# Performance work log

Hardware: AMD Instinct MI355X
Metric: run time of the kernel (lower is better)

Reference implementation:

```python
import jax, jax.numpy as jnp
import numpy as np


def setup_inputs() -> dict:
    key = jax.random.key(0)
    k1, k2 = jax.random.split(key)
    B, H, W, C = 16, 1024, 1024, 3
    image = jax.random.normal(k1, (B, H, W, C), dtype=jnp.float32)
    flow = jax.random.normal(k2, (B, H, W, 2), dtype=jnp.float32)
    return {"image": image, "flow": flow}


def reference(image, flow):
    # Backward warp: out(p) = bilinear_sample(image, p + flow(p)).
    # NOTE: the original build() swaps width/height (width=shape[1], height=shape[2]);
    # this is only consistent for square images (H == W), which we assume here.
    B, H, W, C = image.shape
    grid_x = jnp.arange(W, dtype=jnp.float32)[None, None, :]  # [1,1,W]
    grid_y = jnp.arange(H, dtype=jnp.float32)[None, :, None]  # [1,H,1]
    x = grid_x + flow[..., 0]  # [B,H,W]
    y = grid_y + flow[..., 1]
    # normalize to [-1,1] then back (faithful to original round-trip)
    x = 0.5 * (2.0 * (x / W - 0.5) + 1.0) * W
    y = 0.5 * (2.0 * (y / H - 0.5) + 1.0) * H
    # corner indices (tf.cast truncates toward zero, as does astype(int32))
    x0 = x.astype(jnp.int32)
    x1 = x0 + 1
    y0 = y.astype(jnp.int32)
    y1 = y0 + 1
    x0 = jnp.clip(x0, 0, W - 1)
    x1 = jnp.clip(x1, 0, W - 1)
    y0 = jnp.clip(y0, 0, H - 1)
    y1 = jnp.clip(y1, 0, H - 1)
    # flat gather indices into [B*H*W, C] image, matching the 4 tf.gather calls
    base = (jnp.arange(B, dtype=jnp.int32) * (H * W))[:, None, None]  # [B,1,1]
    flat_img = image.reshape(B * H * W, C)
    ia = (base + y0 * W + x0).reshape(-1)
    ib = (base + y1 * W + x0).reshape(-1)
    ic = (base + y0 * W + x1).reshape(-1)
    idd = (base + y1 * W + x1).reshape(-1)
    pa = flat_img[ia]  # [B*H*W, C]
    pb = flat_img[ib]
    pc = flat_img[ic]
    pd = flat_img[idd]
    # bilinear blend weights from clipped corner coords (as in original)
    x0f = x0.astype(jnp.float32).reshape(-1)
    x1f = x1.astype(jnp.float32).reshape(-1)
    y0f = y0.astype(jnp.float32).reshape(-1)
    y1f = y1.astype(jnp.float32).reshape(-1)
    xf = x.reshape(-1)
    yf = y.reshape(-1)
    wa = ((x1f - xf) * (y1f - yf))[:, None]
    wb = ((x1f - xf) * (yf - y0f))[:, None]
    wc = ((xf - x0f) * (y1f - yf))[:, None]
    wd = ((xf - x0f) * (yf - y0f))[:, None]
    out = wa * pa + wb * pb + wc * pc + wd * pd
    return out.reshape(B, H, W, C)
```

## Files before the change

kernel.cpp:

```cpp
#include <hip/hip_runtime.h>


__global__ __launch_bounds__(256) void backwarp_kernel(
    const float* __restrict__ image,
    const float* __restrict__ flow,
    float* __restrict__ out,
    int B, int H, int W) {
  int idx = blockIdx.x * blockDim.x + threadIdx.x;
  int total = B * H * W;
  if (idx >= total) return;

  int w  = idx % W;
  int hw = idx / W;
  int h  = hw % H;
  int b  = hw / H;

  float2 f = *reinterpret_cast<const float2*>(flow + (size_t)idx * 2);

  float Wf = (float)W, Hf = (float)H;
  float x = (float)w + f.x;
  float y = (float)h + f.y;
  x = 0.5f * (2.0f * (x / Wf - 0.5f) + 1.0f) * Wf;
  y = 0.5f * (2.0f * (y / Hf - 0.5f) + 1.0f) * Hf;

  int x0 = (int)x;
  int y0 = (int)y;
  int x1 = x0 + 1;
  int y1 = y0 + 1;
  x0 = min(max(x0, 0), W - 1);
  x1 = min(max(x1, 0), W - 1);
  y0 = min(max(y0, 0), H - 1);
  y1 = min(max(y1, 0), H - 1);

  float x0f = (float)x0, x1f = (float)x1;
  float y0f = (float)y0, y1f = (float)y1;
  float wa = (x1f - x) * (y1f - y);
  float wb = (x1f - x) * (y - y0f);
  float wc = (x - x0f) * (y1f - y);
  float wd = (x - x0f) * (y - y0f);

  size_t plane = (size_t)b * H * W;
  const float* pa = image + (plane + (size_t)y0 * W + x0) * 3;
  const float* pb = image + (plane + (size_t)y1 * W + x0) * 3;
  const float* pc = image + (plane + (size_t)y0 * W + x1) * 3;
  const float* pd = image + (plane + (size_t)y1 * W + x1) * 3;

  float* o = out + (size_t)idx * 3;
#pragma unroll
  for (int c = 0; c < 3; ++c) {
    o[c] = wa * pa[c] + wb * pb[c] + wc * pc[c] + wd * pd[c];
  }
}

extern "C" void kernel_launch(void* const* d_in, const int* in_sizes, int n_in,
                              void* d_out, int out_size, void* d_ws, size_t ws_size,
                              hipStream_t stream) {
  const float* image = (const float*)d_in[0];
  const float* flow  = (const float*)d_in[1];
  float* out = (float*)d_out;

  const int B = 16, H = 1024, W = 1024;
  int total = B * H * W;
  int block = 256;
  int grid = (total + block - 1) / block;
  backwarp_kernel<<<grid, block, 0, stream>>>(image, flow, out, B, H, W);
}
```

Measured before the change: 157.1 us.

## Process four pixels per thread with vectorized flow/output and paired-corner row loads

Each thread now handles four consecutive pixels, loading flow with two float4 reads and writing output with three float4 stores. The four corner gathers become two 6-float row loads per pixel (x0 and x0+1 together), with selects handling the clamped edge. Dimensions are hardcoded as constants, replacing divisions and modulos with shifts and masks. This cuts memory instruction count and index math, at the cost of more registers per thread and a kernel tied to the fixed shape.

Result: slower. 247.7 us (+57.7%).

```diff
diff --git a/kernel.cpp b/kernel.cpp
--- a/kernel.cpp
+++ b/kernel.cpp
@@ -1,55 +1,68 @@
 #include <hip/hip_runtime.h>
 
+
+struct __attribute__((packed, aligned(4))) R6 { float v[6]; };
 
 __global__ __launch_bounds__(256) void backwarp_kernel(
     const float* __restrict__ image,
     const float* __restrict__ flow,
-    float* __restrict__ out,
-    int B, int H, int W) {
-  int idx = blockIdx.x * blockDim.x + threadIdx.x;
-  int total = B * H * W;
-  if (idx >= total) return;
+    float* __restrict__ out) {
+  constexpr int H = 1024, W = 1024;
+  int t = blockIdx.x * blockDim.x + threadIdx.x;
+  int p0 = t << 2;
+  int w0 = p0 & (W - 1);
+  int h  = (p0 >> 10) & (H - 1);
+  int b  = p0 >> 20;
+  int plane = b << 20;
 
-  int w  = idx % W;
-  int hw = idx / W;
-  int h  = hw % H;
-  int b  = hw / H;
+  const float4 fA = *reinterpret_cast<const float4*>(flow + (size_t)p0 * 2);
+  const float4 fB = *reinterpret_cast<const float4*>(flow + (size_t)p0 * 2 + 4);
+  float fx[4] = {fA.x, fA.z, fB.x, fB.z};
+  float fy[4] = {fA.y, fA.w, fB.y, fB.w};
 
-  float2 f = *reinterpret_cast<const float2*>(flow + (size_t)idx * 2);
+  float res[12];
+#pragma unroll
+  for (int px = 0; px < 4; ++px) {
+    float x = (float)(w0 + px) + fx[px];
+    float y = (float)h + fy[px];
+    x = 0.5f * (2.0f * (x * (1.0f / W) - 0.5f) + 1.0f) * W;
+    y = 0.5f * (2.0f * (y * (1.0f / H) - 0.5f) + 1.0f) * H;
 
-  float Wf = (float)W, Hf = (float)H;
-  float x = (float)w + f.x;
-  float y = (float)h + f.y;
-  x = 0.5f * (2.0f * (x / Wf - 0.5f) + 1.0f) * Wf;
-  y = 0.5f * (2.0f * (y / Hf - 0.5f) + 1.0f) * Hf;
+    int x0 = (int)x;
+    int y0 = (int)y;
+    int x1 = x0 + 1;
+    int y1 = y0 + 1;
+    x0 = min(max(x0, 0), W - 1);
+    x1 = min(max(x1, 0), W - 1);
+    y0 = min(max(y0, 0), H - 1);
+    y1 = min(max(y1, 0), H - 1);
 
-  int x0 = (int)x;
-  int y0 = (int)y;
-  int x1 = x0 + 1;
-  int y1 = y0 + 1;
-  x0 = min(max(x0, 0), W - 1);
-  x1 = min(max(x1, 0), W - 1);
-  y0 = min(max(y0, 0), H - 1);
-  y1 = min(max(y1, 0), H - 1);
+    float wa = ((float)x1 - x) * ((float)y1 - y);
+    float wb = ((float)x1 - x) * (y - (float)y0);
+    float wc = (x - (float)x0) * ((float)y1 - y);
+    float wd = (x - (float)x0) * (y - (float)y0);
 
-  float x0f = (float)x0, x1f = (float)x1;
-  float y0f = (float)y0, y1f = (float)y1;
-  float wa = (x1f - x) * (y1f - y);
-  float wb = (x1f - x) * (y - y0f);
-  float wc = (x - x0f) * (y1f - y);
-  float wd = (x - x0f) * (y - y0f);
+    int bx = min(x0, W - 2);
+    bool hiA = (x0 != bx);
+    bool hiC = (x1 != bx);
 
-  size_t plane = (size_t)b * H * W;
-  const float* pa = image + (plane + (size_t)y0 * W + x0) * 3;
-  const float* pb = image + (plane + (size_t)y1 * W + x0) * 3;
-  const float* pc = image + (plane + (size_t)y0 * W + x1) * 3;
-  const float* pd = image + (plane + (size_t)y1 * W + x1) * 3;
+    const R6 r0 = *reinterpret_cast<const R6*>(image + (size_t)(plane + (y0 << 10) + bx) * 3);
+    const R6 r1 = *reinterpret_cast<const R6*>(image + (size_t)(plane + (y1 << 10) + bx) * 3);
 
-  float* o = out + (size_t)idx * 3;
 #pragma unroll
-  for (int c = 0; c < 3; ++c) {
-    o[c] = wa * pa[c] + wb * pb[c] + wc * pc[c] + wd * pd[c];
+    for (int c = 0; c < 3; ++c) {
+      float pa = hiA ? r0.v[3 + c] : r0.v[c];
+      float pc_ = hiC ? r0.v[3 + c] : r0.v[c];
+      float pb = hiA ? r1.v[3 + c] : r1.v[c];
+      float pd = hiC ? r1.v[3 + c] : r1.v[c];
+      res[px * 3 + c] = wa * pa + wb * pb + wc * pc_ + wd * pd;
+    }
   }
+
+  float4* op = reinterpret_cast<float4*>(out + (size_t)p0 * 3);
+  op[0] = make_float4(res[0], res[1], res[2], res[3]);
+  op[1] = make_float4(res[4], res[5], res[6], res[7]);
+  op[2] = make_float4(res[8], res[9], res[10], res[11]);
 }
 
 extern "C" void kernel_launch(void* const* d_in, const int* in_sizes, int n_in,
@@ -59,9 +72,8 @@
   const float* flow  = (const float*)d_in[1];
   float* out = (float*)d_out;
 
-  const int B = 16, H = 1024, W = 1024;
-  int total = B * H * W;
-  int block = 256;
-  int grid = (total + block - 1) / block;
-  backwarp_kernel<<<grid, block, 0, stream>>>(image, flow, out, B, H, W);
+  const int total = 16 * 1024 * 1024;
+  const int block = 256;
+  const int grid = total / (block * 4);
+  backwarp_kernel<<<grid, block, 0, stream>>>(image, flow, out);
 }
```
